# Optimization experiments

Measured on AMD Instinct MI355X. Metric: run time of the kernel, lower is better.

## Reference

```python
import jax, jax.numpy as jnp
import numpy as np

NV, NF, DIM = 6144, 12288, 256


def _linear(x, W, b):
    # torch nn.Linear: x @ W.T + b, W has shape (out, in)
    return x @ W.T + b


def _agg(X, A, Wf, bf, Wg, bg):
    # AGG: out_fc = Linear(A @ X); out_gagg = Linear(A @ out_fc)  (eval mode: dropout is identity)
    out_fc = _linear(A @ X, Wf, bf)
    out_g = _linear(A @ out_fc, Wg, bg)
    return jax.nn.relu(out_fc + out_g)


def setup_inputs() -> dict:
    key = jax.random.key(0)
    ks = jax.random.split(key, 18)
    primal = jax.random.normal(ks[0], (NV, DIM), jnp.float32)
    # degree-normalized adjacency (docstring): scale uniform entries by 1/N for stable row sums
    A_primal = jax.random.uniform(ks[1], (NV, NV), jnp.float32) * (1.0 / NV)
    A_dual = jax.random.uniform(ks[2], (NF, NF), jnp.float32) * (1.0 / NF)
    A = jax.random.uniform(ks[3], (NV, NF), jnp.float32) * (1.0 / NF)
    faces = jax.random.randint(ks[4], (NF, 3), 0, NV)

    w = lambda k, shp: jax.random.normal(k, shp, jnp.float32) * 0.05
    return {
        "primal": primal, "A_primal": A_primal, "A_dual": A_dual, "A": A, "faces": faces,
        # 3 primal AGG layers (fc + gagg), stacked on leading axis
        "pW": w(ks[5], (3, DIM, DIM)), "pb": w(ks[6], (3, DIM)),
        "pgW": w(ks[7], (3, DIM, DIM)), "pgb": w(ks[8], (3, DIM)),
        # 3 dual AGG layers
        "dW": w(ks[9], (3, DIM, DIM)), "db": w(ks[10], (3, DIM)),
        "dgW": w(ks[11], (3, DIM, DIM)), "dgb": w(ks[12], (3, DIM)),
        # PDF linears: (dim, 2*dim)
        "Wp": w(ks[13], (DIM, 2 * DIM)), "bp": w(ks[14], (DIM,)),
        "Wd": w(ks[15], (DIM, 2 * DIM)), "bd": w(ks[16], (DIM,)),
    }


def reference(primal, A_primal, A_dual, A, faces, pW, pb, pgW, pgb, dW, db, dgW, dgb, Wp, bp, Wd, bd):
    x_p = primal
    x_d = (1.0 / 3.0) * (A.T @ primal)  # primal_dual
    primal_outs, dual_outs = [], []
    for i in range(3):
        primal_outs.append(x_p)
        x_p = _agg(x_p, A_primal, pW[i], pb[i], pgW[i], pgb[i]) + x_p
    for i in range(3):
        dual_outs.append(x_d)
        x_d = _agg(x_d, A_dual, dW[i], db[i], dgW[i], dgb[i]) + x_d
    # PDF: DAP gather-reduce  (N_f, 3, dim) -> (N_f, dim)
    f = jnp.mean(jnp.abs(x_p[faces] - x_d[:, None, :]), axis=1)
    out_dual = jax.nn.relu(_linear(jnp.concatenate([x_d, f], axis=1), Wd, bd))
    mapped = A @ f  # dual_primal
    out_primal = jax.nn.relu(_linear(jnp.concatenate([x_p, mapped], axis=1), Wp, bp))
    return (out_primal + x_p, out_dual + x_d, *primal_outs, *dual_outs)
```

## Files before the change

### kernel.cpp

```cpp
#include <hip/hip_runtime.h>


typedef short short8 __attribute__((ext_vector_type(8)));
typedef float floatx4 __attribute__((ext_vector_type(4)));
typedef unsigned short ushort4v __attribute__((ext_vector_type(4)));
typedef unsigned short u16;

#define DIMN 256
#define GBK 64

static const int kNV = 6144;
static const int kNF = 12288;
static const int SLAB = 768;

__device__ __forceinline__ float bf2f(u16 u) {
  union { unsigned int i; float f; } x; x.i = ((unsigned int)u) << 16; return x.f;
}
__device__ __forceinline__ u16 f2bf(float f) {
  union { float f; unsigned int i; } x; x.f = f;
  unsigned int r = x.i + 0x7fffu + ((x.i >> 16) & 1u);
  return (u16)(r >> 16);
}
__device__ __forceinline__ void gld_lds16(const void* g, void* l) {
  __builtin_amdgcn_global_load_lds((__attribute__((address_space(1))) void*)(g),
                                   (__attribute__((address_space(3))) void*)(l),
                                   16, 0, 0);
}

__global__ __launch_bounds__(256, 2)
void gemm_bf16_k(const void* __restrict__ A0, int A0is32,
                 const void* __restrict__ A1, int A1is32, int K1,
                 int lda0, int lda1,
                 const void* __restrict__ Bt, int Btis32, int ldb,
                 void* __restrict__ P, int M, int nx, int kchunk,
                 int fused, const float* __restrict__ bias,
                 const u16* __restrict__ addmat, int do_relu,
                 const float* __restrict__ resid,
                 float* __restrict__ outf, u16* __restrict__ out16)
{
  __shared__ __align__(16) u16 As[2][128 * GBK];
  __shared__ __align__(16) u16 Bs[2][128 * GBK];

  const int d = blockIdx.x;
  const int y = d & 1;
  const int bx = (d >> 1) % nx;
  const int bz = (d >> 1) / nx;
  const int m0 = bx << 7;
  const int n0 = y << 7;
  const int kb = bz * kchunk;
  const int nkt = kchunk / GBK;

  const int tid = threadIdx.x;
  const int wid = tid >> 6;
  const int lane = tid & 63;
  const int wr = wid >> 1, wc = wid & 1;
  const int srow = lane >> 3;
  const int skk = (lane & 7) << 3;

  floatx4 acc[4][4];
  floatx4 zz = {0.f, 0.f, 0.f, 0.f};
#pragma unroll
  for (int i = 0; i < 4; ++i)
#pragma unroll
    for (int j = 0; j < 4; ++j) acc[i][j] = zz;

  auto stage = [&](int buf, int k0) {
    const void* base; int lda, is32, kl;
    if (k0 < K1) { base = A0; lda = lda0; is32 = A0is32; kl = k0; }
    else         { base = A1; lda = lda1; is32 = A1is32; kl = k0 - K1; }
    if (is32) {
      const float* F = (const float*)base;
#pragma unroll
      for (int j = 0; j < 4; ++j) {
        int c = (wid << 2) + j;
        const size_t gi = (size_t)(m0 + (c << 3) + srow) * lda + kl + skk;
        floatx4 f0 = *(const floatx4*)(F + gi);
        floatx4 f1 = *(const floatx4*)(F + gi + 4);
        short8 v;
#pragma unroll
        for (int e = 0; e < 4; ++e) { v[e] = (short)f2bf(f0[e]); v[4 + e] = (short)f2bf(f1[e]); }
        *(short8*)&As[buf][(c << 9) + (lane << 3)] = v;
      }
    } else {
      const u16* U = (const u16*)base;
#pragma unroll
      for (int j = 0; j < 4; ++j) {
        int c = (wid << 2) + j;
        gld_lds16(U + (size_t)(m0 + (c << 3) + srow) * lda + kl + skk,
                  (void*)&As[buf][c << 9]);
      }
    }
    if (Btis32) {
      const float* F = (const float*)Bt;
#pragma unroll
      for (int j = 0; j < 4; ++j) {
        int c = (wid << 2) + j;
        const size_t gi = (size_t)(n0 + (c << 3) + srow) * ldb + k0 + skk;
        floatx4 f0 = *(const floatx4*)(F + gi);
        floatx4 f1 = *(const floatx4*)(F + gi + 4);
        short8 v;
#pragma unroll
        for (int e = 0; e < 4; ++e) { v[e] = (short)f2bf(f0[e]); v[4 + e] = (short)f2bf(f1[e]); }
        *(short8*)&Bs[buf][(c << 9) + (lane << 3)] = v;
      }
    } else {
      const u16* U = (const u16*)Bt;
#pragma unroll
      for (int j = 0; j < 4; ++j) {
        int c = (wid << 2) + j;
        gld_lds16(U + (size_t)(n0 + (c << 3) + srow) * ldb + k0 + skk,
                  (void*)&Bs[buf][c << 9]);
      }
    }
  };

  int cur = 0;
  stage(0, kb);
  for (int kt = 0; kt < nkt; ++kt) {
    __syncthreads();
    if (kt + 1 < nkt) stage(cur ^ 1, kb + (kt + 1) * GBK);
#pragma unroll
    for (int ks = 0; ks < 2; ++ks) {
      short8 a[4], b[4];
      const int ko = (ks << 5) + ((lane >> 4) << 3);
#pragma unroll
      for (int mi = 0; mi < 4; ++mi)
        a[mi] = *(const short8*)&As[cur][((wr << 6) + (mi << 4) + (lane & 15)) * GBK + ko];
#pragma unroll
      for (int ni = 0; ni < 4; ++ni)
        b[ni] = *(const short8*)&Bs[cur][((wc << 6) + (ni << 4) + (lane & 15)) * GBK + ko];
#pragma unroll
      for (int mi = 0; mi < 4; ++mi)
#pragma unroll
        for (int ni = 0; ni < 4; ++ni)
          acc[mi][ni] = __builtin_amdgcn_mfma_f32_16x16x32_bf16(a[mi], b[ni], acc[mi][ni], 0, 0, 0);
    }
    cur ^= 1;
  }

  if (fused) {
#pragma unroll
    for (int mi = 0; mi < 4; ++mi) {
#pragma unroll
      for (int ni = 0; ni < 4; ++ni) {
        const int mb = m0 + (wr << 6) + (mi << 4) + ((lane >> 4) << 2);
        const int n = n0 + (wc << 6) + (ni << 4) + (lane & 15);
        const float bv = bias ? bias[n] : 0.f;
#pragma unroll
        for (int r = 0; r < 4; ++r) {
          const size_t idx = (size_t)(mb + r) * DIMN + n;
          float t = acc[mi][ni][r] + bv;
          if (addmat) t += bf2f(addmat[idx]);
          if (do_relu) t = fmaxf(t, 0.f);
          if (resid) t += resid[idx];
          if (outf) outf[idx] = t;
          if (out16) out16[idx] = f2bf(t);
        }
      }
    }
  } else {
    u16* Pz = (u16*)P + (size_t)bz * (size_t)M * DIMN;
#pragma unroll
    for (int mi = 0; mi < 4; ++mi) {
#pragma unroll
      for (int ni = 0; ni < 4; ++ni) {
        const int mb = m0 + (wr << 6) + (mi << 4) + ((lane >> 4) << 2);
        const int n = n0 + (wc << 6) + (ni << 4) + (lane & 15);
#pragma unroll
        for (int r = 0; r < 4; ++r)
          Pz[(size_t)(mb + r) * DIMN + n] = f2bf(acc[mi][ni][r]);
      }
    }
  }
}

__global__ __launch_bounds__(256)
void finalize_k(const u16* __restrict__ P, int S, int Mrows, float scale,
                float* __restrict__ out, u16* __restrict__ out16)
{
  const size_t MN = (size_t)Mrows * DIMN;
  const size_t i4 = (((size_t)blockIdx.x * blockDim.x) + threadIdx.x) * 4;
  if (i4 >= MN) return;
  floatx4 v = {0.f, 0.f, 0.f, 0.f};
  for (int s = 0; s < S; ++s) {
    ushort4v p4 = *(const ushort4v*)(P + (size_t)s * MN + i4);
#pragma unroll
    for (int j = 0; j < 4; ++j) v[j] += bf2f(p4[j]);
  }
  floatx4 o;
#pragma unroll
  for (int j = 0; j < 4; ++j) o[j] = v[j] * scale;
  if (out) *(floatx4*)(out + i4) = o;
  if (out16) {
    unsigned long long q = 0;
#pragma unroll
    for (int j = 0; j < 4; ++j) q |= ((unsigned long long)f2bf(o[j])) << (16 * j);
    *(unsigned long long*)(out16 + i4) = q;
  }
}

__global__ __launch_bounds__(256)
void transpose_k(const void* __restrict__ in, int is32, int ldin,
                 u16* __restrict__ out, int ldout, u16* __restrict__ copy16)
{
  __shared__ __align__(16) u16 t[64][64];
  const int c0 = blockIdx.x << 6;
  const int r0 = blockIdx.y << 6;
  const int tid = threadIdx.x;
  const int lr = tid >> 3;
  const int lc = (tid & 7) << 3;
#pragma unroll
  for (int h = 0; h < 2; ++h) {
    const int r = lr + (h << 5);
    short8 v;
    if (is32) {
      const float* F = (const float*)in;
      const size_t gi = (size_t)(r0 + r) * ldin + (c0 + lc);
      floatx4 f0 = *(const floatx4*)(F + gi);
      floatx4 f1 = *(const floatx4*)(F + gi + 4);
#pragma unroll
      for (int e = 0; e < 4; ++e) { v[e] = (short)f2bf(f0[e]); v[4 + e] = (short)f2bf(f1[e]); }
      if (copy16) *(short8*)(copy16 + gi) = v;
    } else {
      v = *(const short8*)((const u16*)in + (size_t)(r0 + r) * ldin + (c0 + lc));
    }
    *(short8*)&t[r][lc ^ ((r >> 3) << 3)] = v;
  }
  __syncthreads();
#pragma unroll
  for (int h = 0; h < 2; ++h) {
    const int oc = lr + (h << 5);
    short8 v;
#pragma unroll
    for (int e = 0; e < 8; ++e)
      v[e] = (short)t[lc + e][oc ^ ((lc >> 3) << 3)];
    *(short8*)&out[(size_t)(c0 + oc) * ldout + (r0 + lc)] = v;
  }
}

__global__ __launch_bounds__(256)
void cvt8_k(const float* __restrict__ in, u16* __restrict__ out, size_t n)
{
  const size_t stride = (size_t)gridDim.x * 2048;
  for (size_t i = (((size_t)blockIdx.x << 8) + threadIdx.x) << 3; i < n; i += stride) {
    floatx4 f0 = *(const floatx4*)(in + i);
    floatx4 f1 = *(const floatx4*)(in + i + 4);
    short8 v;
#pragma unroll
    for (int e = 0; e < 4; ++e) { v[e] = (short)f2bf(f0[e]); v[4 + e] = (short)f2bf(f1[e]); }
    *(short8*)(out + i) = v;
  }
}

__global__ __launch_bounds__(256)
void face_gather_k(const float* __restrict__ xp, const float* __restrict__ xd,
                   const int* __restrict__ faces, u16* __restrict__ f)
{
  const int fi = blockIdx.x;
  const int j = threadIdx.x;
  const int a = faces[fi * 3 + 0];
  const int b = faces[fi * 3 + 1];
  const int c = faces[fi * 3 + 2];
  const float xv = xd[(size_t)fi * DIMN + j];
  const float s = fabsf(xp[(size_t)a * DIMN + j] - xv)
                + fabsf(xp[(size_t)b * DIMN + j] - xv)
                + fabsf(xp[(size_t)c * DIMN + j] - xv);
  f[(size_t)fi * DIMN + j] = f2bf(s * (1.0f / 3.0f));
}

extern "C" void kernel_launch(void* const* d_in, const int* in_sizes, int n_in,
                              void* d_out, int out_size, void* d_ws, size_t ws_size,
                              hipStream_t stream)
{
  (void)in_sizes; (void)n_in; (void)out_size;
  const float* primal   = (const float*)d_in[0];
  const float* A_primal = (const float*)d_in[1];
  const float* A_dual   = (const float*)d_in[2];
  const float* A        = (const float*)d_in[3];
  const int* faces      = (const int*)d_in[4];
  const float* pW  = (const float*)d_in[5];
  const float* pb  = (const float*)d_in[6];
  const float* pgW = (const float*)d_in[7];
  const float* pgb = (const float*)d_in[8];
  const float* dW  = (const float*)d_in[9];
  const float* db  = (const float*)d_in[10];
  const float* dgW = (const float*)d_in[11];
  const float* dgb = (const float*)d_in[12];
  const float* Wp  = (const float*)d_in[13];
  const float* bp  = (const float*)d_in[14];
  const float* Wd  = (const float*)d_in[15];
  const float* bd  = (const float*)d_in[16];

  char* wsp = (char*)d_ws;
  auto alloc = [&](size_t bytes) -> void* {
    void* p = (void*)wsp;
    wsp += (bytes + 255) & ~(size_t)255;
    return p;
  };
  const size_t NVD = (size_t)kNV * DIMN, NFD = (size_t)kNF * DIMN;
  u16* XT    = (u16*)alloc(NFD * 2);
  u16* TB    = (u16*)alloc((size_t)SLAB * kNV * 2);
  u16* t1    = (u16*)alloc(NFD * 2);
  u16* fc    = (u16*)alloc(NFD * 2);
  u16* P     = (u16*)alloc((size_t)8 * NFD * 2);
  const size_t bigElems = (size_t)kNF * kNF + 2 * (size_t)kNF * kNV + (size_t)kNV * kNV;
  const size_t need = (size_t)(wsp - (char*)d_ws) + bigElems * 2 + 4096;
  const bool big = ws_size >= need;
  u16 *Ad16 = nullptr, *At16 = nullptr, *A16 = nullptr, *Ap16 = nullptr;
  if (big) {
    Ad16 = (u16*)alloc((size_t)kNF * kNF * 2);
    At16 = (u16*)alloc((size_t)kNF * kNV * 2);
    A16  = (u16*)alloc((size_t)kNV * kNF * 2);
    Ap16 = (u16*)alloc((size_t)kNV * kNV * 2);
  }

  float* out0  = (float*)d_out;
  float* out1  = out0 + NVD;
  float* pouts = out1 + NFD;
  float* douts = pouts + 3 * NVD;

  auto gemmP = [&](const void* A0p, int a0is32, int lda0,
                   const void* Btp, int ldb, int M, int K, int S) {
    const int nx = M / 128;
    gemm_bf16_k<<<dim3(nx * 2 * S), dim3(256), 0, stream>>>(
        A0p, a0is32, nullptr, 0, K, lda0, 0, Btp, 0, ldb,
        P, M, nx, K / S, 0, nullptr, nullptr, 0, nullptr, nullptr, nullptr);
  };
  auto gemmF = [&](const void* A0p, int a0is32, int lda0,
                   const void* A1p, int a1is32, int lda1, int K1,
                   const float* Btp, int ldb, int M, int K,
                   const float* bias, const u16* add, int relu,
                   const float* resid, float* outf, u16* out16) {
    const int nx = M / 128;
    gemm_bf16_k<<<dim3(nx * 2), dim3(256), 0, stream>>>(
        A0p, a0is32, A1p, a1is32, K1, lda0, lda1, Btp, 1, ldb,
        P, M, nx, K, 1, bias, add, relu, resid, outf, out16);
  };
  auto fin = [&](int M, int S, float scale, float* out, u16* out16) {
    finalize_k<<<dim3((unsigned)((size_t)M * DIMN / 1024)), dim3(256), 0, stream>>>(
        P, S, M, scale, out, out16);
  };
  auto tranp = [&](const void* in, int is32, int ldin, u16* out, int ldout,
                   int R, int C, u16* copy16) {
    transpose_k<<<dim3(C / 64, R / 64), dim3(256), 0, stream>>>(
        in, is32, ldin, out, ldout, copy16);
  };
  auto cvt = [&](const float* in, u16* out, size_t n) {
    cvt8_k<<<dim3(2048), dim3(256), 0, stream>>>(in, out, n);
  };

  if (big) {
    cvt(A_dual, Ad16, (size_t)kNF * kNF);
    cvt(A_primal, Ap16, (size_t)kNV * kNV);
    tranp(A, 1, kNF, At16, kNV, kNV, kNF, A16);
  }

  tranp(primal, 1, DIMN, XT, kNV, kNV, DIMN, nullptr);
  hipMemcpyAsync(pouts, primal, NVD * 4, hipMemcpyDeviceToDevice, stream);

  if (big) {
    gemmP(At16, 0, kNV, XT, kNV, kNF, kNV, 4);
    fin(kNF, 4, 1.0f / 3.0f, douts, nullptr);
  } else {
    for (int s = 0; s < kNF / SLAB; ++s) {
      const int m0 = s * SLAB;
      tranp(A + m0, 1, kNF, TB, kNV, kNV, SLAB, nullptr);
      gemmP(TB, 0, kNV, XT, kNV, SLAB, kNV, 16);
      fin(SLAB, 16, 1.0f / 3.0f, douts + (size_t)m0 * DIMN, nullptr);
    }
  }

  const void* ApP = big ? (const void*)Ap16 : (const void*)A_primal;
  const int apf = big ? 0 : 1;
  const float* xpc = primal;
  for (int i = 0; i < 3; ++i) {
    gemmP(ApP, apf, kNV, XT, kNV, kNV, kNV, 8);
    fin(kNV, 8, 1.f, nullptr, t1);
    gemmF(t1, 0, 256, nullptr, 0, 0, 256, pW + (size_t)i * 65536, 256,
          kNV, 256, pb + i * 256, nullptr, 0, nullptr, nullptr, fc);
    tranp(fc, 0, DIMN, TB, kNV, kNV, DIMN, nullptr);
    gemmP(ApP, apf, kNV, TB, kNV, kNV, kNV, 8);
    fin(kNV, 8, 1.f, nullptr, t1);
    float* nxt = (i < 2) ? (pouts + (size_t)(i + 1) * NVD) : out0;
    gemmF(t1, 0, 256, nullptr, 0, 0, 256, pgW + (size_t)i * 65536, 256,
          kNV, 256, pgb + i * 256, fc, 1, xpc, nxt, nullptr);
    xpc = nxt;
    if (i < 2) tranp(xpc, 1, DIMN, XT, kNV, kNV, DIMN, nullptr);
  }

  const void* AdP = big ? (const void*)Ad16 : (const void*)A_dual;
  const int adf = big ? 0 : 1;
  const float* xdc = douts;
  tranp(xdc, 1, DIMN, XT, kNF, kNF, DIMN, nullptr);
  for (int i = 0; i < 3; ++i) {
    gemmP(AdP, adf, kNF, XT, kNF, kNF, kNF, 4);
    fin(kNF, 4, 1.f, nullptr, t1);
    gemmF(t1, 0, 256, nullptr, 0, 0, 256, dW + (size_t)i * 65536, 256,
          kNF, 256, db + i * 256, nullptr, 0, nullptr, nullptr, fc);
    tranp(fc, 0, DIMN, TB, kNF, kNF, DIMN, nullptr);
    gemmP(AdP, adf, kNF, TB, kNF, kNF, kNF, 4);
    fin(kNF, 4, 1.f, nullptr, t1);
    float* nxt = (i < 2) ? (douts + (size_t)(i + 1) * NFD) : out1;
    gemmF(t1, 0, 256, nullptr, 0, 0, 256, dgW + (size_t)i * 65536, 256,
          kNF, 256, dgb + i * 256, fc, 1, xdc, nxt, nullptr);
    xdc = nxt;
    if (i < 2) tranp(xdc, 1, DIMN, XT, kNF, kNF, DIMN, nullptr);
  }

  face_gather_k<<<dim3(kNF), dim3(256), 0, stream>>>(xpc, xdc, faces, t1);
  tranp(t1, 0, DIMN, TB, kNF, kNF, DIMN, nullptr);
  gemmF(xdc, 1, 256, t1, 0, 256, 256, Wd, 512, kNF, 512,
        bd, nullptr, 1, xdc, out1, nullptr);
  if (big) gemmP(A16, 0, kNF, TB, kNF, kNV, kNF, 8);
  else     gemmP(A, 1, kNF, TB, kNF, kNV, kNF, 8);
  fin(kNV, 8, 1.f, nullptr, fc);
  gemmF(xpc, 1, 256, fc, 0, 256, 256, Wp, 512, kNV, 512,
        bp, nullptr, 1, xpc, out0, nullptr);
}
```

Measured before the change: 2.127 ms.

## Fold split-K partial reduction into the following linear GEMM via replicated weights

Drops the finalize kernels that summed split-K partial slabs. The following linear GEMM now reads the partial slabs directly as a longer K dimension, using bf16 weight copies replicated once per slab, packed into an arena by a new repw_k kernel. It also adds a finalize kernel that writes the initial dual features together with their bf16 transpose, reorders the primal and dual stages, and remaps block indices for locality. This removes launches and intermediate round trips, at the cost of larger-K linear GEMMs (1024–2304 instead of 256) and bf16 rounding of the partial sums before they are accumulated.

```diff
diff --git a/kernel.cpp b/kernel.cpp
--- a/kernel.cpp
+++ b/kernel.cpp
@@ -13,6 +13,13 @@
 static const int kNF = 12288;
 static const int SLAB = 768;
 
+#define RW_PW    0
+#define RW_PGW   1572864
+#define RW_DW    3145728
+#define RW_DGW   3932160
+#define RW_WCOMB 4718592
+#define RW_TOT   5308416
+
 __device__ __forceinline__ float bf2f(u16 u) {
   union { unsigned int i; float f; } x; x.i = ((unsigned int)u) << 16; return x.f;
 }
@@ -28,8 +35,8 @@
 }
 
 __global__ __launch_bounds__(256, 2)
-void gemm_bf16_k(const void* __restrict__ A0, int A0is32,
-                 const void* __restrict__ A1, int A1is32, int K1,
+void gemm_bf16_k(const void* __restrict__ A0, int A0is32, size_t aslab0,
+                 const void* __restrict__ A1, int A1is32, size_t aslab1, int K1,
                  int lda0, int lda1,
                  const void* __restrict__ Bt, int Btis32, int ldb,
                  void* __restrict__ P, int M, int nx, int kchunk,
@@ -41,7 +48,8 @@
   __shared__ __align__(16) u16 As[2][128 * GBK];
   __shared__ __align__(16) u16 Bs[2][128 * GBK];
 
-  const int d = blockIdx.x;
+  const int nwg = gridDim.x;
+  const int d = ((blockIdx.x & 7) * (nwg >> 3)) + (blockIdx.x >> 3);
   const int y = d & 1;
   const int bx = (d >> 1) % nx;
   const int bz = (d >> 1) / nx;
@@ -65,15 +73,16 @@
     for (int j = 0; j < 4; ++j) acc[i][j] = zz;
 
   auto stage = [&](int buf, int k0) {
-    const void* base; int lda, is32, kl;
-    if (k0 < K1) { base = A0; lda = lda0; is32 = A0is32; kl = k0; }
-    else         { base = A1; lda = lda1; is32 = A1is32; kl = k0 - K1; }
+    const void* base; int lda, is32, kl; size_t aslab;
+    if (k0 < K1) { base = A0; lda = lda0; is32 = A0is32; kl = k0; aslab = aslab0; }
+    else { base = A1; lda = lda1; is32 = A1is32; kl = k0 - K1; aslab = aslab1; }
+    const size_t koff = aslab ? ((size_t)(kl >> 8) * aslab + (kl & 255)) : (size_t)kl;
     if (is32) {
       const float* F = (const float*)base;
 #pragma unroll
       for (int j = 0; j < 4; ++j) {
         int c = (wid << 2) + j;
-        const size_t gi = (size_t)(m0 + (c << 3) + srow) * lda + kl + skk;
+        const size_t gi = (size_t)(m0 + (c << 3) + srow) * lda + koff + skk;
         floatx4 f0 = *(const floatx4*)(F + gi);
         floatx4 f1 = *(const floatx4*)(F + gi + 4);
         short8 v;
@@ -86,7 +95,7 @@
 #pragma unroll
       for (int j = 0; j < 4; ++j) {
         int c = (wid << 2) + j;
-        gld_lds16(U + (size_t)(m0 + (c << 3) + srow) * lda + kl + skk,
+        gld_lds16(U + (size_t)(m0 + (c << 3) + srow) * lda + koff + skk,
                   (void*)&As[buf][c << 9]);
       }
     }
@@ -200,6 +209,52 @@
 }
 
 __global__ __launch_bounds__(256)
+void finalize_tr_k(const u16* __restrict__ P, int S, int Mrows, float scale,
+                   float* __restrict__ outf, u16* __restrict__ outT, int ldT)
+{
+  __shared__ __align__(16) u16 t[64][64];
+  const size_t MN = (size_t)Mrows * DIMN;
+  const int r0 = blockIdx.x << 6;
+  const int c0 = blockIdx.y << 6;
+  const int tid = threadIdx.x;
+  const int lr = tid >> 3;
+  const int lc = (tid & 7) << 3;
+#pragma unroll
+  for (int h = 0; h < 2; ++h) {
+    const int r = lr + (h << 5);
+    const size_t gi = (size_t)(r0 + r) * DIMN + (c0 + lc);
+    float a[8];
+#pragma unroll
+    for (int e = 0; e < 8; ++e) a[e] = 0.f;
+    for (int s = 0; s < S; ++s) {
+      short8 p = *(const short8*)(P + (size_t)s * MN + gi);
+#pragma unroll
+      for (int e = 0; e < 8; ++e) a[e] += bf2f((u16)p[e]);
+    }
+    short8 v;
+    floatx4 o0, o1;
+#pragma unroll
+    for (int e = 0; e < 4; ++e) {
+      o0[e] = a[e] * scale; o1[e] = a[4 + e] * scale;
+      v[e] = (short)f2bf(o0[e]); v[4 + e] = (short)f2bf(o1[e]);
+    }
+    *(floatx4*)(outf + gi) = o0;
+    *(floatx4*)(outf + gi + 4) = o1;
+    *(short8*)&t[r][lc ^ ((r >> 3) << 3)] = v;
+  }
+  __syncthreads();
+#pragma unroll
+  for (int h = 0; h < 2; ++h) {
+    const int oc = lr + (h << 5);
+    short8 v;
+#pragma unroll
+    for (int e = 0; e < 8; ++e)
+      v[e] = (short)t[lc + e][oc ^ ((lc >> 3) << 3)];
+    *(short8*)&outT[(size_t)(c0 + oc) * ldT + (r0 + lc)] = v;
+  }
+}
+
+__global__ __launch_bounds__(256)
 void transpose_k(const void* __restrict__ in, int is32, int ldin,
                  u16* __restrict__ out, int ldout, u16* __restrict__ copy16)
 {
@@ -250,6 +305,37 @@
     for (int e = 0; e < 4; ++e) { v[e] = (short)f2bf(f0[e]); v[4 + e] = (short)f2bf(f1[e]); }
     *(short8*)(out + i) = v;
   }
+}
+
+__global__ __launch_bounds__(256)
+void repw_k(const float* __restrict__ pW, const float* __restrict__ pgW,
+            const float* __restrict__ dW, const float* __restrict__ dgW,
+            const float* __restrict__ Wp, u16* __restrict__ arena)
+{
+  const size_t o = (((size_t)blockIdx.x << 8) + threadIdx.x) << 3;
+  if (o >= RW_TOT) return;
+  const float* src;
+  size_t so;
+  if (o < RW_PGW) {
+    size_t r = o - RW_PW; int i = (int)(r >> 19); int rr = (int)(r & 524287);
+    so = (size_t)i * 65536 + (rr >> 11) * 256 + (rr & 255); src = pW;
+  } else if (o < RW_DW) {
+    size_t r = o - RW_PGW; int i = (int)(r >> 19); int rr = (int)(r & 524287);
+    so = (size_t)i * 65536 + (rr >> 11) * 256 + (rr & 255); src = pgW;
+  } else if (o < RW_DGW) {
+    size_t r = o - RW_DW; int i = (int)(r >> 18); int rr = (int)(r & 262143);
+    so = (size_t)i * 65536 + (rr >> 10) * 256 + (rr & 255); src = dW;
+  } else if (o < RW_WCOMB) {
+    size_t r = o - RW_DGW; int i = (int)(r >> 18); int rr = (int)(r & 262143);
+    so = (size_t)i * 65536 + (rr >> 10) * 256 + (rr & 255); src = dgW;
+  } else {
+    size_t r = o - RW_WCOMB; int n = (int)(r / 2304); int k2 = (int)(r % 2304);
+    so = (size_t)n * 512 + ((k2 < 256) ? k2 : (256 + ((k2 - 256) & 255))); src = Wp;
+  }
+  short8 v;
+#pragma unroll
+  for (int e = 0; e < 8; ++e) v[e] = (short)f2bf(src[so + e]);
+  *(short8*)(arena + o) = v;
 }
 
 __global__ __launch_bounds__(256)
@@ -303,6 +389,7 @@
   u16* t1    = (u16*)alloc(NFD * 2);
   u16* fc    = (u16*)alloc(NFD * 2);
   u16* P     = (u16*)alloc((size_t)8 * NFD * 2);
+  u16* Wrep  = (u16*)alloc((size_t)RW_TOT * 2);
   const size_t bigElems = (size_t)kNF * kNF + 2 * (size_t)kNF * kNV + (size_t)kNV * kNV;
   const size_t need = (size_t)(wsp - (char*)d_ws) + bigElems * 2 + 4096;
   const bool big = ws_size >= need;
@@ -323,22 +410,18 @@
                    const void* Btp, int ldb, int M, int K, int S) {
     const int nx = M / 128;
     gemm_bf16_k<<<dim3(nx * 2 * S), dim3(256), 0, stream>>>(
-        A0p, a0is32, nullptr, 0, K, lda0, 0, Btp, 0, ldb,
+        A0p, a0is32, 0, nullptr, 0, 0, K, lda0, 0, Btp, 0, ldb,
         P, M, nx, K / S, 0, nullptr, nullptr, 0, nullptr, nullptr, nullptr);
   };
-  auto gemmF = [&](const void* A0p, int a0is32, int lda0,
-                   const void* A1p, int a1is32, int lda1, int K1,
-                   const float* Btp, int ldb, int M, int K,
+  auto gemmF = [&](const void* A0p, int a0is32, size_t as0, int lda0,
+                   const void* A1p, int a1is32, size_t as1, int lda1, int K1,
+                   const void* Btp, int btis32, int ldb, int M, int K,
                    const float* bias, const u16* add, int relu,
                    const float* resid, float* outf, u16* out16) {
     const int nx = M / 128;
     gemm_bf16_k<<<dim3(nx * 2), dim3(256), 0, stream>>>(
-        A0p, a0is32, A1p, a1is32, K1, lda0, lda1, Btp, 1, ldb,
+        A0p, a0is32, as0, A1p, a1is32, as1, K1, lda0, lda1, Btp, btis32, ldb,
         P, M, nx, K, 1, bias, add, relu, resid, outf, out16);
-  };
-  auto fin = [&](int M, int S, float scale, float* out, u16* out16) {
-    finalize_k<<<dim3((unsigned)((size_t)M * DIMN / 1024)), dim3(256), 0, stream>>>(
-        P, S, M, scale, out, out16);
   };
   auto tranp = [&](const void* in, int is32, int ldin, u16* out, int ldout,
                    int R, int C, u16* copy16) {
@@ -349,71 +432,76 @@
     cvt8_k<<<dim3(2048), dim3(256), 0, stream>>>(in, out, n);
   };
 
+  repw_k<<<dim3(RW_TOT / 2048), dim3(256), 0, stream>>>(pW, pgW, dW, dgW, Wp, Wrep);
   if (big) {
     cvt(A_dual, Ad16, (size_t)kNF * kNF);
     cvt(A_primal, Ap16, (size_t)kNV * kNV);
     tranp(A, 1, kNF, At16, kNV, kNV, kNF, A16);
   }
-
   tranp(primal, 1, DIMN, XT, kNV, kNV, DIMN, nullptr);
   hipMemcpyAsync(pouts, primal, NVD * 4, hipMemcpyDeviceToDevice, stream);
 
+  const void* ApP = big ? (const void*)Ap16 : (const void*)A_primal;
+  const int apf = big ? 0 : 1;
+  const void* AdP = big ? (const void*)Ad16 : (const void*)A_dual;
+  const int adf = big ? 0 : 1;
+
+  const float* xpc = primal;
+  for (int i = 0; i < 3; ++i) {
+    gemmP(ApP, apf, kNV, XT, kNV, kNV, kNV, 8);
+    gemmF(P, 0, NVD, 256, nullptr, 0, 0, 0, 2048,
+          Wrep + RW_PW + (size_t)i * 524288, 0, 2048, kNV, 2048,
+          pb + i * 256, nullptr, 0, nullptr, nullptr, fc);
+    tranp(fc, 0, DIMN, TB, kNV, kNV, DIMN, nullptr);
+    gemmP(ApP, apf, kNV, TB, kNV, kNV, kNV, 8);
+    float* nxt = (i < 2) ? (pouts + (size_t)(i + 1) * NVD) : out0;
+    gemmF(P, 0, NVD, 256, nullptr, 0, 0, 0, 2048,
+          Wrep + RW_PGW + (size_t)i * 524288, 0, 2048, kNV, 2048,
+          pgb + i * 256, fc, 1, xpc, nxt, nullptr);
+    xpc = nxt;
+    if (i < 2) tranp(xpc, 1, DIMN, XT, kNV, kNV, DIMN, nullptr);
+  }
+
   if (big) {
+    tranp(primal, 1, DIMN, XT, kNV, kNV, DIMN, nullptr);
     gemmP(At16, 0, kNV, XT, kNV, kNF, kNV, 4);
-    fin(kNF, 4, 1.0f / 3.0f, douts, nullptr);
+    finalize_tr_k<<<dim3(kNF / 64, 4), dim3(256), 0, stream>>>(
+        P, 4, kNF, 1.0f / 3.0f, douts, XT, kNF);
   } else {
+    tranp(primal, 1, DIMN, XT, kNV, kNV, DIMN, nullptr);
     for (int s = 0; s < kNF / SLAB; ++s) {
       const int m0 = s * SLAB;
       tranp(A + m0, 1, kNF, TB, kNV, kNV, SLAB, nullptr);
       gemmP(TB, 0, kNV, XT, kNV, SLAB, kNV, 16);
-      fin(SLAB, 16, 1.0f / 3.0f, douts + (size_t)m0 * DIMN, nullptr);
-    }
-  }
-
-  const void* ApP = big ? (const void*)Ap16 : (const void*)A_primal;
-  const int apf = big ? 0 : 1;
-  const float* xpc = primal;
-  for (int i = 0; i < 3; ++i) {
-    gemmP(ApP, apf, kNV, XT, kNV, kNV, kNV, 8);
-    fin(kNV, 8, 1.f, nullptr, t1);
-    gemmF(t1, 0, 256, nullptr, 0, 0, 256, pW + (size_t)i * 65536, 256,
-          kNV, 256, pb + i * 256, nullptr, 0, nullptr, nullptr, fc);
-    tranp(fc, 0, DIMN, TB, kNV, kNV, DIMN, nullptr);
-    gemmP(ApP, apf, kNV, TB, kNV, kNV, kNV, 8);
-    fin(kNV, 8, 1.f, nullptr, t1);
-    float* nxt = (i < 2) ? (pouts + (size_t)(i + 1) * NVD) : out0;
-    gemmF(t1, 0, 256, nullptr, 0, 0, 256, pgW + (size_t)i * 65536, 256,
-          kNV, 256, pgb + i * 256, fc, 1, xpc, nxt, nullptr);
-    xpc = nxt;
-    if (i < 2) tranp(xpc, 1, DIMN, XT, kNV, kNV, DIMN, nullptr);
-  }
-
-  const void* AdP = big ? (const void*)Ad16 : (const void*)A_dual;
-  const int adf = big ? 0 : 1;
+      finalize_k<<<dim3((unsigned)((size_t)SLAB * DIMN / 1024)), dim3(256), 0, stream>>>(
+          P, 16, SLAB, 1.0f / 3.0f, douts + (size_t)m0 * DIMN, nullptr);
+    }
+    tranp(douts, 1, DIMN, XT, kNF, kNF, DIMN, nullptr);
+  }
+
   const float* xdc = douts;
-  tranp(xdc, 1, DIMN, XT, kNF, kNF, DIMN, nullptr);
   for (int i = 0; i < 3; ++i) {
     gemmP(AdP, adf, kNF, XT, kNF, kNF, kNF, 4);
-    fin(kNF, 4, 1.f, nullptr, t1);
-    gemmF(t1, 0, 256, nullptr, 0, 0, 256, dW + (size_t)i * 65536, 256,
-          kNF, 256, db + i * 256, nullptr, 0, nullptr, nullptr, fc);
+    gemmF(P, 0, NFD, 256, nullptr, 0, 0, 0, 1024,
+          Wrep + RW_DW + (size_t)i * 262144, 0, 1024, kNF, 1024,
+          db + i * 256, nullptr, 0, nullptr, nullptr, fc);
     tranp(fc, 0, DIMN, TB, kNF, kNF, DIMN, nullptr);
     gemmP(AdP, adf, kNF, TB, kNF, kNF, kNF, 4);
-    fin(kNF, 4, 1.f, nullptr, t1);
     float* nxt = (i < 2) ? (douts + (size_t)(i + 1) * NFD) : out1;
-    gemmF(t1, 0, 256, nullptr, 0, 0, 256, dgW + (size_t)i * 65536, 256,
-          kNF, 256, dgb + i * 256, fc, 1, xdc, nxt, nullptr);
+    gemmF(P, 0, NFD, 256, nullptr, 0, 0, 0, 1024,
+          Wrep + RW_DGW + (size_t)i * 262144, 0, 1024, kNF, 1024,
+          dgb + i * 256, fc, 1, xdc, nxt, nullptr);
     xdc = nxt;
     if (i < 2) tranp(xdc, 1, DIMN, XT, kNF, kNF, DIMN, nullptr);
   }
 
   face_gather_k<<<dim3(kNF), dim3(256), 0, stream>>>(xpc, xdc, faces, t1);
   tranp(t1, 0, DIMN, TB, kNF, kNF, DIMN, nullptr);
-  gemmF(xdc, 1, 256, t1, 0, 256, 256, Wd, 512, kNF, 512,
+  gemmF(xdc, 1, 0, 256, t1, 0, 0, 256, 256, Wd, 1, 512, kNF, 512,
         bd, nullptr, 1, xdc, out1, nullptr);
   if (big) gemmP(A16, 0, kNF, TB, kNF, kNV, kNF, 8);
   else     gemmP(A, 1, kNF, TB, kNF, kNV, kNF, 8);
-  fin(kNV, 8, 1.f, nullptr, fc);
-  gemmF(xpc, 1, 256, fc, 0, 256, 256, Wp, 512, kNV, 512,
+  gemmF(xpc, 1, 0, 256, P, 0, NVD, 256, 256,
+        Wrep + RW_WCOMB, 0, 2304, kNV, 2304,
         bp, nullptr, 1, xpc, out0, nullptr);
 }
```

Result: slower. 2.206 ms (+3.7%).
